# Performance work log

Hardware: AMD Instinct MI355X
Metric: run time of the kernel (lower is better)

The kernel has to match this reference:

```python
import jax, jax.numpy as jnp
import numpy as np

N_TYPES = 2
N_NODES = 50000
N_EDGES = 400000
C = 128
H = 4
D = C // H
L = 2
# edge type e connects src node type META[e][0] -> dst node type META[e][1]
META = ((0, 1), (1, 0))


def setup_inputs() -> dict:
    key = jax.random.key(0)
    ks = jax.random.split(key, 16)
    s = 0.05
    return {
        "x": jax.random.normal(ks[0], (N_TYPES, N_NODES, C), jnp.float32),
        "edge_index": jax.random.randint(ks[1], (2, 2, N_EDGES), 0, N_NODES, jnp.int64),
        "Wk": jax.random.normal(ks[2], (L, N_TYPES, C, C), jnp.float32) * s,
        "bk": jax.random.normal(ks[3], (L, N_TYPES, C), jnp.float32) * s,
        "Wq": jax.random.normal(ks[4], (L, N_TYPES, C, C), jnp.float32) * s,
        "bq": jax.random.normal(ks[5], (L, N_TYPES, C), jnp.float32) * s,
        "Wv": jax.random.normal(ks[6], (L, N_TYPES, C, C), jnp.float32) * s,
        "bv": jax.random.normal(ks[7], (L, N_TYPES, C), jnp.float32) * s,
        "Wa": jax.random.normal(ks[8], (L, N_TYPES, C, C), jnp.float32) * s,
        "ba": jax.random.normal(ks[9], (L, N_TYPES, C), jnp.float32) * s,
        "skip": jax.random.normal(ks[10], (L, N_TYPES), jnp.float32),
        "a_rel": jax.random.normal(ks[11], (L, 2, H, D, D), jnp.float32) * s,
        "m_rel": jax.random.normal(ks[12], (L, 2, H, D, D), jnp.float32) * s,
        "p_rel": jnp.ones((L, 2, H), jnp.float32),
        "ln_g": jnp.ones((L, N_TYPES, C), jnp.float32),
        "ln_b": jnp.zeros((L, N_TYPES, C), jnp.float32),
    }


def _layer(x, edge_index, Wk, bk, Wq, bq, Wv, bv, Wa, ba, skip, a_rel, m_rel, p_rel, ln_g, ln_b):
    # x: [T, N, C] ; per-type K/Q/V projections -> [T, N, H, D]
    k = (jnp.einsum('tnc,tcd->tnd', x, Wk) + bk[:, None]).reshape(N_TYPES, N_NODES, H, D)
    q = (jnp.einsum('tnc,tcd->tnd', x, Wq) + bq[:, None]).reshape(N_TYPES, N_NODES, H, D)
    v = (jnp.einsum('tnc,tcd->tnd', x, Wv) + bv[:, None]).reshape(N_TYPES, N_NODES, H, D)
    scale = 1.0 / float(np.sqrt(D))
    out = jnp.zeros((N_TYPES, N_NODES, H, D), x.dtype)
    for e, (st, dt) in enumerate(META):
        si, di = edge_index[e, 0], edge_index[e, 1]
        # per-relation transforms of gathered src keys/values: [E, H, D]
        k_rel = jnp.einsum('ehd,hdf->ehf', k[st][si], a_rel[e])
        v_rel = jnp.einsum('ehd,hdf->ehf', v[st][si], m_rel[e])
        # attention logits [E, H], softmax grouped by destination node
        att = jnp.sum(q[dt][di] * k_rel, axis=-1) * p_rel[e] * scale
        amax = jax.ops.segment_max(att, di, num_segments=N_NODES)
        att = jnp.exp(att - amax[di])
        den = jax.ops.segment_sum(att, di, num_segments=N_NODES)
        att = att / (den[di] + 1e-16)
        agg = jax.ops.segment_sum(att[..., None] * v_rel, di, num_segments=N_NODES)
        out = out.at[dt].add(agg)
    o = out.reshape(N_TYPES, N_NODES, C)
    o = jnp.einsum('tnc,tcd->tnd', jax.nn.gelu(o), Wa) + ba[:, None]
    beta = jax.nn.sigmoid(skip)[:, None, None]
    x = beta * o + (1.0 - beta) * x
    # per-type LayerNorm over features, then ReLU
    mu = jnp.mean(x, axis=-1, keepdims=True)
    var = jnp.var(x, axis=-1, keepdims=True)
    x = (x - mu) * jax.lax.rsqrt(var + 1e-5) * ln_g[:, None] + ln_b[:, None]
    return jax.nn.relu(x)


def reference(x, edge_index, Wk, bk, Wq, bq, Wv, bv, Wa, ba, skip, a_rel, m_rel, p_rel, ln_g, ln_b):
    for l in range(L):
        x = _layer(x, edge_index, Wk[l], bk[l], Wq[l], bq[l], Wv[l], bv[l],
                   Wa[l], ba[l], skip[l], a_rel[l], m_rel[l], p_rel[l], ln_g[l], ln_b[l])
    # x_dict[entity_table]: return node type 0 ("user") embeddings
    return x[0]
```

## Files before the change

kernel.cpp:

```cpp
#include <hip/hip_runtime.h>

#define NN 50000
#define EE 400000
#define CC 128
#define TT 2
#define NT16R 3128
#define KPB 8

typedef float floatx4 __attribute__((ext_vector_type(4)));
typedef float floatx2 __attribute__((ext_vector_type(2)));
typedef _Float16 half8 __attribute__((ext_vector_type(8)));
typedef _Float16 half2t __attribute__((ext_vector_type(2)));

__device__ __forceinline__ unsigned pk2h(float a, float b) {
    return __builtin_bit_cast(unsigned, __builtin_amdgcn_cvt_pkrtz(a, b));
}
__device__ __forceinline__ float gelu_f(float x) {
    float u = 0.7978845608028654f * (x + 0.044715f * x * x * x);
    float t = __expf(2.f * u);
    return x * (1.f - 1.f / (t + 1.f));
}

__device__ __forceinline__ floatx2 pkfma(floatx2 a, floatx2 b, floatx2 c) {
#if __has_builtin(__builtin_elementwise_fma)
    return __builtin_elementwise_fma(a, b, c);
#else
    floatx2 r;
    r.x = fmaf(a.x, b.x, c.x);
    r.y = fmaf(a.y, b.y, c.y);
    return r;
#endif
}

__device__ __forceinline__ unsigned pk_fp8x4(float a, float b, float c, float d) {
#if __has_builtin(__builtin_amdgcn_cvt_pk_fp8_f32)
    int v = 0;
    v = __builtin_amdgcn_cvt_pk_fp8_f32(a, b, v, false);
    v = __builtin_amdgcn_cvt_pk_fp8_f32(c, d, v, true);
    return (unsigned)v;
#else
    auto enc = [](float x) -> unsigned {
        unsigned u = __float_as_uint(x);
        unsigned s = (u >> 24) & 0x80;
        int e = (int)((u >> 23) & 0xff);
        unsigned m = u & 0x7fffff;
        if (e == 0) return s;
        int ne = e - 127 + 7;
        if (ne <= 0) {
            unsigned full = (1u << 23) | m;
            int sh = 21 - ne;
            if (sh > 24) return s;
            unsigned r = full >> sh;
            unsigned rem = full & ((1u << sh) - 1);
            unsigned half = 1u << (sh - 1);
            if (rem > half || (rem == half && (r & 1))) r++;
            return s | (r & 0x7f);
        }
        unsigned r = m >> 20;
        unsigned rem = m & 0xfffff;
        if (rem > 0x80000 || (rem == 0x80000 && (r & 1))) {
            r++;
            if (r == 8) { r = 0; ne++; }
        }
        if (ne > 15) return s | 0x7e;
        return s | ((unsigned)ne << 3) | r;
    };
    return enc(a) | (enc(b) << 8) | (enc(c) << 16) | (enc(d) << 24);
#endif
}

template <bool HI>
__device__ __forceinline__ floatx2 upk_fp8(unsigned v) {
#if __has_builtin(__builtin_amdgcn_cvt_pk_f32_fp8)
    return __builtin_amdgcn_cvt_pk_f32_fp8((int)v, HI);
#else
    auto dec = [](unsigned b) -> float {
        unsigned s = b & 0x80;
        unsigned e = (b >> 3) & 0xf;
        unsigned m = b & 7;
        float val;
        if (e == 0) val = (float)m * (1.f / 512.f);
        else val = (1.f + (float)m * 0.125f) * exp2f((float)e - 7.f);
        return s ? -val : val;
    };
    unsigned base = HI ? (v >> 16) : v;
    floatx2 r;
    r.x = dec(base & 0xff);
    r.y = dec((base >> 8) & 0xff);
    return r;
#endif
}

__global__ void k_detect(const int* __restrict__ ei, int* __restrict__ flag) {
    if (threadIdx.x == 0 && blockIdx.x == 0) {
        int orv = 0;
        for (int i = 1; i < 64; i += 2) orv |= ei[i];
        flag[0] = (orv == 0) ? 1 : 0;
    }
}

__global__ __launch_bounds__(256) void k_count(const int* __restrict__ ei,
                                               const int* __restrict__ flag,
                                               int* __restrict__ counts,
                                               unsigned short* __restrict__ rank) {
    int e = blockIdx.y;
    int tid = threadIdx.x;
    int base = blockIdx.x * (256 * KPB);
    int is64 = flag[0];
    const size_t db = (size_t)(e * 2 + 1) * EE;
    int di[KPB];
    bool val[KPB];
#pragma unroll
    for (int k = 0; k < KPB; k++) {
        int j = base + k * 256 + tid;
        val[k] = j < EE;
        int jc = val[k] ? j : 0;
        int d = is64 ? ei[(db + jc) * 2] : ei[db + jc];
        di[k] = min(max(d, 0), NN - 1);
    }
    int rk[KPB];
#pragma unroll
    for (int k = 0; k < KPB; k++)
        rk[k] = val[k] ? atomicAdd(&counts[e * NN + di[k]], 1) : 0;
#pragma unroll
    for (int k = 0; k < KPB; k++) {
        int j = base + k * 256 + tid;
        if (val[k]) rank[(size_t)e * EE + j] = (unsigned short)rk[k];
    }
}

#define SCB ((NN + 1023) / 1024)
__global__ __launch_bounds__(256) void k_scan1(const int* __restrict__ counts,
                                               int* __restrict__ rowptr,
                                               int* __restrict__ bsum) {
    int e = blockIdx.y, b = blockIdx.x;
    int tid = threadIdx.x, lane = tid & 63, wid = tid >> 6;
    __shared__ int wsum[4];
    int base = b * 1024 + tid * 4;
    int v[4], s = 0;
#pragma unroll
    for (int k2 = 0; k2 < 4; k2++) {
        int i = base + k2;
        v[k2] = (i < NN) ? counts[e * NN + i] : 0;
        s += v[k2];
    }
    int incl = s;
#pragma unroll
    for (int off = 1; off < 64; off <<= 1) {
        int t2 = __shfl_up(incl, off);
        if (lane >= off) incl += t2;
    }
    if (lane == 63) wsum[wid] = incl;
    __syncthreads();
    int woff = 0;
    for (int w2 = 0; w2 < wid; w2++) woff += wsum[w2];
    int excl = woff + incl - s;
#pragma unroll
    for (int k2 = 0; k2 < 4; k2++) {
        int i = base + k2;
        if (i < NN) rowptr[e * (NN + 1) + i] = excl;
        excl += v[k2];
    }
    if (tid == 255) bsum[e * SCB + b] = woff + incl;
}

__global__ void k_scan2(int* __restrict__ bsum, int* __restrict__ rowptr) {
    int e = threadIdx.x >> 6, lane = threadIdx.x & 63;
    int v = (lane < SCB) ? bsum[e * SCB + lane] : 0;
    int incl = v;
#pragma unroll
    for (int off = 1; off < 64; off <<= 1) {
        int t2 = __shfl_up(incl, off);
        if (lane >= off) incl += t2;
    }
    if (lane < SCB) bsum[e * SCB + lane] = incl - v;
    if (lane == 63) rowptr[e * (NN + 1) + NN] = incl;
}

__global__ __launch_bounds__(256) void k_scan3(int* __restrict__ rowptr,
                                               const int* __restrict__ bsum) {
    int e = blockIdx.y, b = blockIdx.x;
    int off = bsum[e * SCB + b];
    int base = b * 1024 + threadIdx.x * 4;
#pragma unroll
    for (int k2 = 0; k2 < 4; k2++) {
        int i = base + k2;
        if (i < NN) rowptr[e * (NN + 1) + i] += off;
    }
}

__global__ __launch_bounds__(256) void k_scatter(const int* __restrict__ ei,
                                                 const int* __restrict__ flag,
                                                 const int* __restrict__ rowptr,
                                                 const unsigned short* __restrict__ rank,
                                                 int* __restrict__ csr) {
    int e = blockIdx.y;
    int tid = threadIdx.x;
    int base = blockIdx.x * (256 * KPB);
    int is64 = flag[0];
    const size_t sb = (size_t)(e * 2 + 0) * EE;
    const size_t db = (size_t)(e * 2 + 1) * EE;
    int si[KPB], di[KPB], rk[KPB];
#pragma unroll
    for (int k = 0; k < KPB; k++) {
        int j = base + k * 256 + tid;
        int jc = (j < EE) ? j : 0;
        si[k] = is64 ? ei[(sb + jc) * 2] : ei[sb + jc];
        di[k] = is64 ? ei[(db + jc) * 2] : ei[db + jc];
        rk[k] = rank[(size_t)e * EE + jc];
    }
    int pos[KPB];
#pragma unroll
    for (int k = 0; k < KPB; k++) {
        di[k] = min(max(di[k], 0), NN - 1);
        si[k] = min(max(si[k], 0), NN - 1);
    }
#pragma unroll
    for (int k = 0; k < KPB; k++) pos[k] = rowptr[e * (NN + 1) + di[k]] + rk[k];
#pragma unroll
    for (int k = 0; k < KPB; k++) {
        int j = base + k * 256 + tid;
        if (j < EE) csr[(size_t)e * EE + pos[k]] = si[k];
    }
}

__global__ __launch_bounds__(256) void k_cvt(const float* __restrict__ x,
                                             _Float16* __restrict__ xs) {
    __shared__ _Float16 sm[64 * 132];
    int t = blockIdx.y;
    int tid = threadIdx.x;
    int node0 = blockIdx.x * 64;
#pragma unroll
    for (int p = 0; p < 8; p++) {
        int c = p * 256 + tid;
        int row = c >> 5, ch = c & 31;
        int node = min(node0 + row, NN - 1);
        float4 v = *(const float4*)(x + ((size_t)t * NN + node) * CC + ch * 4);
        uint2 o;
        o.x = pk2h(v.x, v.y);
        o.y = pk2h(v.z, v.w);
        *(uint2*)(sm + row * 132 + ch * 4) = o;
    }
    __syncthreads();
    _Float16* xt = xs + (size_t)t * NT16R * 2048;
#pragma unroll
    for (int p = 0; p < 4; p++) {
        int c = p * 256 + tid;
        int tl = c >> 8, kt = (c >> 6) & 3, l = c & 63;
        int q = l >> 4, ln = l & 15;
        *(uint4*)(xt + ((size_t)(blockIdx.x * 4 + tl) * 4 + kt) * 512 + l * 8) =
            *(const uint4*)(sm + (tl * 16 + ln) * 132 + kt * 32 + q * 8);
    }
}

__global__ void k_prep(const float* __restrict__ Wk, const float* __restrict__ Wq,
                       const float* __restrict__ Wv, const float* __restrict__ Wa,
                       const float* __restrict__ bk, const float* __restrict__ bq,
                       const float* __restrict__ bv,
                       const float* __restrict__ a_rel, const float* __restrict__ m_rel,
                       const float* __restrict__ p_rel,
                       _Float16* __restrict__ W2, _Float16* __restrict__ Wa2,
                       float* __restrict__ beff) {
    const float SCALE = 0.17677669529663687f * 1.4426950408889634f;
    int l = blockIdx.y;
    int idx = blockIdx.x * 256 + threadIdx.x;
    if (idx < 2 * 384 * 128) {
        int t = idx / (384 * 128);
        int r = idx - t * 384 * 128;
        int n = r >> 7, k = r & 127;
        float val;
        if (n < 128) {
            val = Wq[((l * 2 + t) * 128 + k) * 128 + n] *
                  p_rel[(l * 2 + (1 - t)) * 4 + (n >> 5)] * SCALE;
        } else if (n < 256) {
            int nn = n - 128, h = nn >> 5, f = nn & 31;
            const float* wr = Wk + ((l * 2 + t) * 128 + k) * 128 + h * 32;
            const float* ar = a_rel + (((l * 2 + t) * 4 + h) * 32) * 32 + f;
            float s = 0.f;
            for (int d = 0; d < 32; d++) s += wr[d] * ar[d * 32];
            val = s;
        } else {
            int nn = n - 256, h = nn >> 5, f = nn & 31;
            const float* wr = Wv + ((l * 2 + t) * 128 + k) * 128 + h * 32;
            const float* mr = m_rel + (((l * 2 + t) * 4 + h) * 32) * 32 + f;
            float s = 0.f;
            for (int d = 0; d < 32; d++) s += wr[d] * mr[d * 32];
            val = s;
        }
        W2[(((size_t)(l * 2 + t) * 24 + (n >> 4)) * 4 + (k >> 5)) * 512 +
           (((k & 31) >> 3) * 16 + (n & 15)) * 8 + (k & 7)] = (_Float16)val;
    } else if (idx < 2 * 384 * 128 + 2 * 128 * 128) {
        int r = idx - 2 * 384 * 128;
        int t = r / (128 * 128);
        r -= t * 128 * 128;
        int n = r >> 7, k = r & 127;
        float val = Wa[((l * 2 + t) * 128 + k) * 128 + n];
        Wa2[(((size_t)(l * 2 + t) * 8 + (n >> 4)) * 4 + (k >> 5)) * 512 +
            (((k & 31) >> 3) * 16 + (n & 15)) * 8 + (k & 7)] = (_Float16)val;
    } else if (idx < 2 * 384 * 128 + 2 * 128 * 128 + 2 * 384) {
        int r = idx - (2 * 384 * 128 + 2 * 128 * 128);
        int t = r / 384, n = r - t * 384;
        float val;
        if (n < 128) {
            val = bq[(l * 2 + t) * 128 + n] * p_rel[(l * 2 + (1 - t)) * 4 + (n >> 5)] * SCALE;
        } else if (n < 256) {
            int nn = n - 128, h = nn >> 5, f = nn & 31;
            float s = 0.f;
            for (int d = 0; d < 32; d++)
                s += bk[(l * 2 + t) * 128 + h * 32 + d] *
                     a_rel[(((l * 2 + t) * 4 + h) * 32 + d) * 32 + f];
            val = s;
        } else {
            int nn = n - 256, h = nn >> 5, f = nn & 31;
            float s = 0.f;
            for (int d = 0; d < 32; d++)
                s += bv[(l * 2 + t) * 128 + h * 32 + d] *
                     m_rel[(((l * 2 + t) * 4 + h) * 32 + d) * 32 + f];
            val = s;
        }
        beff[(l * 2 + t) * 384 + n] = val;
    }
}

template <int NT, int COL0>
__global__ __launch_bounds__(256) void k_gemm_qkv(const _Float16* __restrict__ xs,
                                                  const _Float16* __restrict__ W2,
                                                  const float* __restrict__ beff,
                                                  unsigned char* __restrict__ qkv8, int l,
                                                  int t0) {
    constexpr int RB = (NT == 6) ? 512 : 256;
    constexpr int RS = RB + 16;
    __shared__ unsigned char tile[32 * RS];
    int t = t0 + blockIdx.y;
    int tid = threadIdx.x;
    int wid = tid >> 6, lane = tid & 63;
    int quad = lane >> 4, ln = lane & 15;
    int node0 = blockIdx.x * 32;
    int tile0 = blockIdx.x * 2;
    int lt = l * 2 + t;
    const _Float16* Wt = W2 + (size_t)lt * 24 * 2048;
    const _Float16* xt = xs + (size_t)t * NT16R * 2048;
    half8 bf[2][4];
#pragma unroll
    for (int ns = 0; ns < 2; ns++)
#pragma unroll
        for (int kt = 0; kt < 4; kt++)
            bf[ns][kt] = *(const half8*)(xt + ((size_t)(tile0 + ns) * 4 + kt) * 512 + lane * 8);
    floatx4 acc[NT][2];
#pragma unroll
    for (int nt = 0; nt < NT; nt++)
#pragma unroll
        for (int ns = 0; ns < 2; ns++) acc[nt][ns] = (floatx4){0.f, 0.f, 0.f, 0.f};
#pragma unroll
    for (int nt = 0; nt < NT; nt++) {
        int mt = COL0 / 16 + wid * NT + nt;
#pragma unroll
        for (int kt = 0; kt < 4; kt++) {
            half8 af = *(const half8*)(Wt + ((size_t)mt * 4 + kt) * 512 + lane * 8);
            acc[nt][0] = __builtin_amdgcn_mfma_f32_16x16x32_f16(af, bf[0][kt], acc[nt][0], 0, 0, 0);
            acc[nt][1] = __builtin_amdgcn_mfma_f32_16x16x32_f16(af, bf[1][kt], acc[nt][1], 0, 0, 0);
        }
    }
#pragma unroll
    for (int nt = 0; nt < NT; nt++) {
        int c0 = COL0 + wid * NT * 16 + nt * 16 + quad * 4;
        float4 b4 = *(const float4*)(beff + (l * 2 + t) * 384 + c0);
#pragma unroll
        for (int ns = 0; ns < 2; ns++) {
            int nl = ns * 16 + ln;
            float v0 = acc[nt][ns][0] + b4.x, v1 = acc[nt][ns][1] + b4.y;
            float v2 = acc[nt][ns][2] + b4.z, v3 = acc[nt][ns][3] + b4.w;
            unsigned char* rowp = tile + nl * RS;
            if (c0 < 128) {
                uint2 o;
                o.x = pk2h(v0, v1);
                o.y = pk2h(v2, v3);
                *(uint2*)(rowp + 2 * c0) = o;
            } else {
                int f0 = c0 & 127;
                int isV = (c0 >= 256);
                int loff = (f0 >> 3) * 16 + (f0 & 7) + isV * 8 +
                           ((COL0 == 128) ? 0 : 256);
                *(unsigned*)(rowp + loff) = pk_fp8x4(v0, v1, v2, v3);
            }
        }
    }
    __syncthreads();
    constexpr int CPR = RB / 16;
    constexpr int PASSES = (32 * CPR) / 256;
#pragma unroll
    for (int p = 0; p < PASSES; p++) {
        int c = p * 256 + tid;
        int row = c / CPR, ch = c - row * CPR;
        int node = node0 + row;
        if (node < NN)
            *(uint4*)(qkv8 + ((size_t)t * NN + node) * 512 + (COL0 ? 256 : 0) + ch * 16) =
                *(const uint4*)(tile + row * RS + ch * 16);
    }
}

__global__ __launch_bounds__(256) void k_attn(const unsigned char* __restrict__ qkv8,
                                              const int* __restrict__ rowptr,
                                              const int* __restrict__ csr,
                                              _Float16* __restrict__ outg) {
    int t = blockIdx.y;
    int e = 1 - t;
    int st = 1 - t;
    int wid = threadIdx.x >> 6, lane = threadIdx.x & 63;
    int n = __builtin_amdgcn_readfirstlane(blockIdx.x * 4 + wid);
    int e4 = lane >> 4, s = lane & 15;
    int r0 = rowptr[e * (NN + 1) + n];
    int r1 = rowptr[e * (NN + 1) + n + 1];
    const int* csrp = csr + (size_t)e * EE;
    const unsigned char* sbase = qkv8 + (size_t)st * NN * 512;
    uint4 qd = *(const uint4*)(qkv8 + ((size_t)t * NN + n) * 512 + s * 16);

    floatx2 acc2[4];
#pragma unroll
    for (int i = 0; i < 4; i++) acc2[i] = (floatx2){0.f, 0.f};
    float lsum = 0.f;
    floatx2 q2[4];

    auto process = [&](const uint4& u, float msk) {
        floatx2 p2 = q2[0] * upk_fp8<false>(u.x);
        p2 = pkfma(q2[1], upk_fp8<true>(u.x), p2);
        p2 = pkfma(q2[2], upk_fp8<false>(u.y), p2);
        p2 = pkfma(q2[3], upk_fp8<true>(u.y), p2);
        float p = p2.x + p2.y;
        p += __shfl_xor(p, 1);
        p += __shfl_xor(p, 2);
        float w = exp2f(p) * msk;
        lsum += w;
        floatx2 w2 = (floatx2){w, w};
        acc2[0] = pkfma(w2, upk_fp8<false>(u.z), acc2[0]);
        acc2[1] = pkfma(w2, upk_fp8<true>(u.z), acc2[1]);
        acc2[2] = pkfma(w2, upk_fp8<false>(u.w), acc2[2]);
        acc2[3] = pkfma(w2, upk_fp8<true>(u.w), acc2[3]);
    };

    if (r0 < r1) {
        int j = r0;
        int iA = csrp[min(j + e4, r1 - 1)];
        int iB = csrp[min(j + 4 + e4, r1 - 1)];
        uint4 uA = (uint4){0u, 0u, 0u, 0u};
        if (j + e4 < r1) uA = *(const uint4*)(sbase + (size_t)iA * 512 + 256 + s * 16);
        {
            half2t h0 = __builtin_bit_cast(half2t, qd.x), h1 = __builtin_bit_cast(half2t, qd.y);
            half2t h2 = __builtin_bit_cast(half2t, qd.z), h3 = __builtin_bit_cast(half2t, qd.w);
            q2[0] = (floatx2){(float)h0.x, (float)h0.y};
            q2[1] = (floatx2){(float)h1.x, (float)h1.y};
            q2[2] = (floatx2){(float)h2.x, (float)h2.y};
            q2[3] = (floatx2){(float)h3.x, (float)h3.y};
        }
        for (; j + 8 < r1; j += 4) {
            uint4 uB = *(const uint4*)(sbase + (size_t)iB * 512 + 256 + s * 16);
            iB = csrp[min(j + 8 + e4, r1 - 1)];
            process(uA, 1.f);
            uA = uB;
        }
        if (j + 4 < r1) {
            uint4 uB = (uint4){0u, 0u, 0u, 0u};
            float mB = (j + 4 + e4 < r1) ? 1.f : 0.f;
            if (j + 4 + e4 < r1)
                uB = *(const uint4*)(sbase + (size_t)iB * 512 + 256 + s * 16);
            process(uA, 1.f);
            process(uB, mB);
        } else {
            process(uA, (j + e4 < r1) ? 1.f : 0.f);
        }
    }
    float accf[8] = {acc2[0].x, acc2[0].y, acc2[1].x, acc2[1].y,
                     acc2[2].x, acc2[2].y, acc2[3].x, acc2[3].y};
#pragma unroll
    for (int i = 0; i < 8; i++) {
        accf[i] += __shfl_xor(accf[i], 16);
        accf[i] += __shfl_xor(accf[i], 32);
    }
    lsum += __shfl_xor(lsum, 16);
    lsum += __shfl_xor(lsum, 32);
    float inv = 1.f / (lsum + 1e-16f);
    if (e4 == 0) {
        uint4 o;
        o.x = pk2h(accf[0] * inv, accf[1] * inv);
        o.y = pk2h(accf[2] * inv, accf[3] * inv);
        o.z = pk2h(accf[4] * inv, accf[5] * inv);
        o.w = pk2h(accf[6] * inv, accf[7] * inv);
        *(uint4*)(outg + ((size_t)t * NN + n) * CC + s * 8) = o;
    }
}

__global__ __launch_bounds__(256) void k_epilogue(
    const _Float16* __restrict__ outg, const _Float16* __restrict__ Wa2,
    const float* __restrict__ ba, const float* __restrict__ skipv,
    const float* __restrict__ ln_g, const float* __restrict__ ln_b,
    const _Float16* __restrict__ xs_cur, _Float16* __restrict__ xs_next,
    float* __restrict__ xout, int l) {
    __shared__ _Float16 smem_h[64 * 132];
    int t = blockIdx.y;
    int tid = threadIdx.x;
    int wid = tid >> 6, lane = tid & 63;
    int quad = lane >> 4, ln = lane & 15;
    int node0 = blockIdx.x * 64;
    int nloc = wid * 16 + ln;
    int node = node0 + nloc;
    int arow = min(node, NN - 1);
    const _Float16* grow = outg + ((size_t)t * NN + arow) * CC;
    uint4 gd4[4];
#pragma unroll
    for (int kt = 0; kt < 4; kt++) gd4[kt] = *(const uint4*)(grow + kt * 32 + quad * 8);
    const _Float16* xt = xs_cur + (size_t)t * NT16R * 2048;
    int tileR = arow >> 4, lnR = arow & 15;
    uint2 xw8[8];
#pragma unroll
    for (int nt = 0; nt < 8; nt++) {
        int c0 = nt * 16 + quad * 4;
        xw8[nt] = *(const uint2*)(xt + ((size_t)tileR * 4 + (c0 >> 5)) * 512 +
                                  (((c0 >> 3) & 3) * 16 + lnR) * 8 + (c0 & 7));
    }
    half8 bf[4];
#pragma unroll
    for (int kt = 0; kt < 4; kt++) {
        uint4 gd = gd4[kt];
        half2t h0 = __builtin_bit_cast(half2t, gd.x), h1 = __builtin_bit_cast(half2t, gd.y);
        half2t h2 = __builtin_bit_cast(half2t, gd.z), h3 = __builtin_bit_cast(half2t, gd.w);
        uint4 pk;
        pk.x = pk2h(gelu_f((float)h0.x), gelu_f((float)h0.y));
        pk.y = pk2h(gelu_f((float)h1.x), gelu_f((float)h1.y));
        pk.z = pk2h(gelu_f((float)h2.x), gelu_f((float)h2.y));
        pk.w = pk2h(gelu_f((float)h3.x), gelu_f((float)h3.y));
        bf[kt] = __builtin_bit_cast(half8, pk);
    }
    const _Float16* Wt = Wa2 + (size_t)(l * 2 + t) * 8 * 2048;
    floatx4 acc[8];
#pragma unroll
    for (int nt = 0; nt < 8; nt++) acc[nt] = (floatx4){0.f, 0.f, 0.f, 0.f};
#pragma unroll
    for (int nt = 0; nt < 8; nt++) {
#pragma unroll
        for (int kt = 0; kt < 4; kt++) {
            half8 af = *(const half8*)(Wt + ((size_t)nt * 4 + kt) * 512 + lane * 8);
            acc[nt] = __builtin_amdgcn_mfma_f32_16x16x32_f16(af, bf[kt], acc[nt], 0, 0, 0);
        }
    }
    float sv = skipv[l * TT + t];
    float beta = 1.f / (1.f + __expf(-sv));
    float xn[8][4];
    float s1 = 0.f, s2 = 0.f;
#pragma unroll
    for (int nt = 0; nt < 8; nt++) {
        int c0 = nt * 16 + quad * 4;
        float4 b4 = *(const float4*)(ba + (l * TT + t) * CC + c0);
        half2t x0 = __builtin_bit_cast(half2t, xw8[nt].x),
               x1 = __builtin_bit_cast(half2t, xw8[nt].y);
        float xv[4] = {(float)x0.x, (float)x0.y, (float)x1.x, (float)x1.y};
        float bb[4] = {b4.x, b4.y, b4.z, b4.w};
#pragma unroll
        for (int reg = 0; reg < 4; reg++) {
            float o = acc[nt][reg] + bb[reg];
            float v = beta * o + (1.f - beta) * xv[reg];
            xn[nt][reg] = v;
            s1 += v;
            s2 += v * v;
        }
    }
    s1 += __shfl_xor(s1, 16); s1 += __shfl_xor(s1, 32);
    s2 += __shfl_xor(s2, 16); s2 += __shfl_xor(s2, 32);
    float mu = s1 * (1.f / CC);
    float var = s2 * (1.f / CC) - mu * mu;
    float rs = rsqrtf(var + 1e-5f);
#pragma unroll
    for (int nt = 0; nt < 8; nt++) {
        int c0 = nt * 16 + quad * 4;
        float4 g4 = *(const float4*)(ln_g + (l * TT + t) * CC + c0);
        float4 be4 = *(const float4*)(ln_b + (l * TT + t) * CC + c0);
        float y0 = fmaxf((xn[nt][0] - mu) * rs * g4.x + be4.x, 0.f);
        float y1 = fmaxf((xn[nt][1] - mu) * rs * g4.y + be4.y, 0.f);
        float y2 = fmaxf((xn[nt][2] - mu) * rs * g4.z + be4.z, 0.f);
        float y3 = fmaxf((xn[nt][3] - mu) * rs * g4.w + be4.w, 0.f);
        if (xout) {
            if (node < NN) {
                float4 o4 = {y0, y1, y2, y3};
                *(float4*)(xout + (size_t)node * CC + c0) = o4;
            }
        } else {
            uint2 o;
            o.x = pk2h(y0, y1);
            o.y = pk2h(y2, y3);
            *(uint2*)(smem_h + nloc * 132 + c0) = o;
        }
    }
    if (!xout) {
        __syncthreads();
        _Float16* xnt = xs_next + (size_t)t * NT16R * 2048;
#pragma unroll
        for (int p = 0; p < 4; p++) {
            int c = p * 256 + tid;
            int tl = c >> 8, kt2 = (c >> 6) & 3, l2 = c & 63;
            int q2 = l2 >> 4, ln2 = l2 & 15;
            *(uint4*)(xnt + ((size_t)(blockIdx.x * 4 + tl) * 4 + kt2) * 512 + l2 * 8) =
                *(const uint4*)(smem_h + (tl * 16 + ln2) * 132 + kt2 * 32 + q2 * 8);
        }
    }
}

extern "C" void kernel_launch(void* const* d_in, const int* in_sizes, int n_in,
                              void* d_out, int out_size, void* d_ws, size_t ws_size,
                              hipStream_t stream) {
    const float* x = (const float*)d_in[0];
    const int* ei = (const int*)d_in[1];
    const float* Wk = (const float*)d_in[2];
    const float* bk = (const float*)d_in[3];
    const float* Wq = (const float*)d_in[4];
    const float* bq = (const float*)d_in[5];
    const float* Wv = (const float*)d_in[6];
    const float* bv = (const float*)d_in[7];
    const float* Wa = (const float*)d_in[8];
    const float* ba = (const float*)d_in[9];
    const float* skip = (const float*)d_in[10];
    const float* a_rel = (const float*)d_in[11];
    const float* m_rel = (const float*)d_in[12];
    const float* p_rel = (const float*)d_in[13];
    const float* ln_g = (const float*)d_in[14];
    const float* ln_b = (const float*)d_in[15];

    char* ws = (char*)d_ws;
    size_t off = 0;
    auto alloc = [&](size_t b) {
        size_t o = off;
        off = (off + b + 255) & ~(size_t)255;
        return o;
    };
    _Float16* xsA = (_Float16*)(ws + alloc((size_t)TT * NT16R * 2048 * 2));
    _Float16* xsB = (_Float16*)(ws + alloc((size_t)TT * NT16R * 2048 * 2));
    unsigned char* qkv8 = (unsigned char*)(ws + alloc((size_t)TT * NN * 512));
    _Float16* outg = (_Float16*)(ws + alloc((size_t)TT * NN * CC * 2));
    _Float16* W2 = (_Float16*)(ws + alloc((size_t)2 * TT * 24 * 2048 * 2));
    _Float16* Wa2 = (_Float16*)(ws + alloc((size_t)2 * TT * 8 * 2048 * 2));
    float* beff = (float*)(ws + alloc((size_t)2 * TT * 384 * 4));
    int* counts = (int*)(ws + alloc((size_t)2 * NN * 4));
    unsigned short* rankb = (unsigned short*)(ws + alloc((size_t)2 * EE * 2));
    int* rowptr = (int*)(ws + alloc((size_t)2 * (NN + 1) * 4));
    int* csr = (int*)(ws + alloc((size_t)2 * EE * 4));
    int* flag = (int*)(ws + alloc(256));
    int* bsum = (int*)(ws + alloc((size_t)2 * SCB * 4 + 256));
    (void)ws_size; (void)in_sizes; (void)n_in; (void)out_size;

    k_detect<<<1, 64, 0, stream>>>(ei, flag);
    (void)hipMemsetAsync(counts, 0, (size_t)2 * NN * 4, stream);
    const int EB = (EE + 256 * KPB - 1) / (256 * KPB);
    k_count<<<dim3(EB, 2), 256, 0, stream>>>(ei, flag, counts, rankb);
    k_scan1<<<dim3(SCB, 2), 256, 0, stream>>>(counts, rowptr, bsum);
    k_scan2<<<1, 128, 0, stream>>>(bsum, rowptr);
    k_scan3<<<dim3(SCB, 2), 256, 0, stream>>>(rowptr, bsum);
    k_scatter<<<dim3(EB, 2), 256, 0, stream>>>(ei, flag, rowptr, rankb, csr);
    k_cvt<<<dim3(NT16R / 4, 2), 256, 0, stream>>>(x, xsA);
    k_prep<<<dim3((2 * 384 * 128 + 2 * 128 * 128 + 2 * 384 + 255) / 256, 2), 256, 0, stream>>>(
        Wk, Wq, Wv, Wa, bk, bq, bv, a_rel, m_rel, p_rel, W2, Wa2, beff);

    const int GB = (NN + 31) / 32;
    k_gemm_qkv<6, 0><<<dim3(GB, 2), 256, 0, stream>>>(xsA, W2, beff, qkv8, 0, 0);
    k_attn<<<dim3(NN / 4, 2), 256, 0, stream>>>(qkv8, rowptr, csr, outg);
    k_epilogue<<<dim3((NN + 63) / 64, 2), 256, 0, stream>>>(
        outg, Wa2, ba, skip, ln_g, ln_b, xsA, xsB, nullptr, 0);
    k_gemm_qkv<2, 0><<<dim3(GB, 1), 256, 0, stream>>>(xsB, W2, beff, qkv8, 1, 0);
    k_gemm_qkv<4, 128><<<dim3(GB, 1), 256, 0, stream>>>(xsB, W2, beff, qkv8, 1, 1);
    k_attn<<<dim3(NN / 4, 1), 256, 0, stream>>>(qkv8, rowptr, csr, outg);
    k_epilogue<<<dim3((NN + 63) / 64, 1), 256, 0, stream>>>(
        outg, Wa2, ba, skip, ln_g, ln_b, xsB, nullptr, (float*)d_out, 1);
}
```

Measured before the change: 332.5 us.

## Merge small launches: inline dtype detect, fuse scan passes, cvt+prep, layer-1 GEMMs

Removes the separate detect kernel by having each count/scatter block check the index dtype itself. The two-pass scan tail becomes a single kernel, and the x conversion and weight prep run as one launch split by block index. The two layer-1 QKV GEMM launches also become one launch over a 2-D grid. The aim is to cut the number of kernel launches and the serialization gaps between them, at the cost of a redundant per-block dtype check and a redundant 64-lane block-sum scan in every scan block.

```diff
diff --git a/kernel.cpp b/kernel.cpp
--- a/kernel.cpp
+++ b/kernel.cpp
@@ -6,6 +6,10 @@
 #define TT 2
 #define NT16R 3128
 #define KPB 8
+#define SCB ((NN + 1023) / 1024)
+#define CVTB (NT16R / 4)
+#define PREPN (2 * 384 * 128 + 2 * 128 * 128 + 2 * 384)
+#define PREPB ((PREPN + 255) / 256)
 
 typedef float floatx4 __attribute__((ext_vector_type(4)));
 typedef float floatx2 __attribute__((ext_vector_type(2)));
@@ -91,22 +95,25 @@
 #endif
 }
 
-__global__ void k_detect(const int* __restrict__ ei, int* __restrict__ flag) {
-    if (threadIdx.x == 0 && blockIdx.x == 0) {
+__device__ __forceinline__ int detect_is64(const int* __restrict__ ei, int* sflag) {
+    if (threadIdx.x == 0) {
         int orv = 0;
+#pragma unroll
         for (int i = 1; i < 64; i += 2) orv |= ei[i];
-        flag[0] = (orv == 0) ? 1 : 0;
-    }
+        *sflag = (orv == 0) ? 1 : 0;
+    }
+    __syncthreads();
+    return *sflag;
 }
 
 __global__ __launch_bounds__(256) void k_count(const int* __restrict__ ei,
-                                               const int* __restrict__ flag,
                                                int* __restrict__ counts,
                                                unsigned short* __restrict__ rank) {
+    __shared__ int sflag;
+    int is64 = detect_is64(ei, &sflag);
     int e = blockIdx.y;
     int tid = threadIdx.x;
     int base = blockIdx.x * (256 * KPB);
-    int is64 = flag[0];
     const size_t db = (size_t)(e * 2 + 1) * EE;
     int di[KPB];
     bool val[KPB];
@@ -129,7 +136,6 @@
     }
 }
 
-#define SCB ((NN + 1023) / 1024)
 __global__ __launch_bounds__(256) void k_scan1(const int* __restrict__ counts,
                                                int* __restrict__ rowptr,
                                                int* __restrict__ bsum) {
@@ -164,40 +170,42 @@
     if (tid == 255) bsum[e * SCB + b] = woff + incl;
 }
 
-__global__ void k_scan2(int* __restrict__ bsum, int* __restrict__ rowptr) {
-    int e = threadIdx.x >> 6, lane = threadIdx.x & 63;
-    int v = (lane < SCB) ? bsum[e * SCB + lane] : 0;
-    int incl = v;
-#pragma unroll
-    for (int off = 1; off < 64; off <<= 1) {
-        int t2 = __shfl_up(incl, off);
-        if (lane >= off) incl += t2;
-    }
-    if (lane < SCB) bsum[e * SCB + lane] = incl - v;
-    if (lane == 63) rowptr[e * (NN + 1) + NN] = incl;
-}
-
-__global__ __launch_bounds__(256) void k_scan3(int* __restrict__ rowptr,
-                                               const int* __restrict__ bsum) {
+__global__ __launch_bounds__(256) void k_scan23(int* __restrict__ rowptr,
+                                                const int* __restrict__ bsum) {
+    __shared__ int soff2[2];
     int e = blockIdx.y, b = blockIdx.x;
-    int off = bsum[e * SCB + b];
-    int base = b * 1024 + threadIdx.x * 4;
+    int tid = threadIdx.x, lane = tid & 63, wv = tid >> 6;
+    if (wv == 0) {
+        int v = (lane < SCB) ? bsum[e * SCB + lane] : 0;
+        int incl = v;
+#pragma unroll
+        for (int off = 1; off < 64; off <<= 1) {
+            int t2 = __shfl_up(incl, off);
+            if (lane >= off) incl += t2;
+        }
+        if (lane == b) soff2[0] = incl - v;
+        if (lane == SCB - 1) soff2[1] = incl;
+    }
+    __syncthreads();
+    int off = soff2[0];
+    int base = b * 1024 + tid * 4;
 #pragma unroll
     for (int k2 = 0; k2 < 4; k2++) {
         int i = base + k2;
         if (i < NN) rowptr[e * (NN + 1) + i] += off;
     }
+    if (b == 0 && tid == 0) rowptr[e * (NN + 1) + NN] = soff2[1];
 }
 
 __global__ __launch_bounds__(256) void k_scatter(const int* __restrict__ ei,
-                                                 const int* __restrict__ flag,
                                                  const int* __restrict__ rowptr,
                                                  const unsigned short* __restrict__ rank,
                                                  int* __restrict__ csr) {
+    __shared__ int sflag;
+    int is64 = detect_is64(ei, &sflag);
     int e = blockIdx.y;
     int tid = threadIdx.x;
     int base = blockIdx.x * (256 * KPB);
-    int is64 = flag[0];
     const size_t sb = (size_t)(e * 2 + 0) * EE;
     const size_t db = (size_t)(e * 2 + 1) * EE;
     int si[KPB], di[KPB], rk[KPB];
@@ -224,46 +232,48 @@
     }
 }
 
-__global__ __launch_bounds__(256) void k_cvt(const float* __restrict__ x,
-                                             _Float16* __restrict__ xs) {
+__global__ __launch_bounds__(256) void k_cvt_prep(
+    const float* __restrict__ x, _Float16* __restrict__ xs,
+    const float* __restrict__ Wk, const float* __restrict__ Wq,
+    const float* __restrict__ Wv, const float* __restrict__ Wa,
+    const float* __restrict__ bk, const float* __restrict__ bq,
+    const float* __restrict__ bv,
+    const float* __restrict__ a_rel, const float* __restrict__ m_rel,
+    const float* __restrict__ p_rel,
+    _Float16* __restrict__ W2, _Float16* __restrict__ Wa2,
+    float* __restrict__ beff) {
     __shared__ _Float16 sm[64 * 132];
-    int t = blockIdx.y;
     int tid = threadIdx.x;
-    int node0 = blockIdx.x * 64;
-#pragma unroll
-    for (int p = 0; p < 8; p++) {
-        int c = p * 256 + tid;
-        int row = c >> 5, ch = c & 31;
-        int node = min(node0 + row, NN - 1);
-        float4 v = *(const float4*)(x + ((size_t)t * NN + node) * CC + ch * 4);
-        uint2 o;
-        o.x = pk2h(v.x, v.y);
-        o.y = pk2h(v.z, v.w);
-        *(uint2*)(sm + row * 132 + ch * 4) = o;
-    }
-    __syncthreads();
-    _Float16* xt = xs + (size_t)t * NT16R * 2048;
-#pragma unroll
-    for (int p = 0; p < 4; p++) {
-        int c = p * 256 + tid;
-        int tl = c >> 8, kt = (c >> 6) & 3, l = c & 63;
-        int q = l >> 4, ln = l & 15;
-        *(uint4*)(xt + ((size_t)(blockIdx.x * 4 + tl) * 4 + kt) * 512 + l * 8) =
-            *(const uint4*)(sm + (tl * 16 + ln) * 132 + kt * 32 + q * 8);
-    }
-}
-
-__global__ void k_prep(const float* __restrict__ Wk, const float* __restrict__ Wq,
-                       const float* __restrict__ Wv, const float* __restrict__ Wa,
-                       const float* __restrict__ bk, const float* __restrict__ bq,
-                       const float* __restrict__ bv,
-                       const float* __restrict__ a_rel, const float* __restrict__ m_rel,
-                       const float* __restrict__ p_rel,
-                       _Float16* __restrict__ W2, _Float16* __restrict__ Wa2,
-                       float* __restrict__ beff) {
+    if (blockIdx.x < CVTB) {
+        int bx = blockIdx.x;
+        int t = blockIdx.y;
+        int node0 = bx * 64;
+#pragma unroll
+        for (int p = 0; p < 8; p++) {
+            int c = p * 256 + tid;
+            int row = c >> 5, ch = c & 31;
+            int node = min(node0 + row, NN - 1);
+            float4 v = *(const float4*)(x + ((size_t)t * NN + node) * CC + ch * 4);
+            uint2 o;
+            o.x = pk2h(v.x, v.y);
+            o.y = pk2h(v.z, v.w);
+            *(uint2*)(sm + row * 132 + ch * 4) = o;
+        }
+        __syncthreads();
+        _Float16* xt = xs + (size_t)t * NT16R * 2048;
+#pragma unroll
+        for (int p = 0; p < 4; p++) {
+            int c = p * 256 + tid;
+            int tl = c >> 8, kt = (c >> 6) & 3, l = c & 63;
+            int q = l >> 4, ln = l & 15;
+            *(uint4*)(xt + ((size_t)(bx * 4 + tl) * 4 + kt) * 512 + l * 8) =
+                *(const uint4*)(sm + (tl * 16 + ln) * 132 + kt * 32 + q * 8);
+        }
+        return;
+    }
     const float SCALE = 0.17677669529663687f * 1.4426950408889634f;
     int l = blockIdx.y;
-    int idx = blockIdx.x * 256 + threadIdx.x;
+    int idx = (blockIdx.x - CVTB) * 256 + tid;
     if (idx < 2 * 384 * 128) {
         int t = idx / (384 * 128);
         int r = idx - t * 384 * 128;
@@ -297,7 +307,7 @@
         float val = Wa[((l * 2 + t) * 128 + k) * 128 + n];
         Wa2[(((size_t)(l * 2 + t) * 8 + (n >> 4)) * 4 + (k >> 5)) * 512 +
             (((k & 31) >> 3) * 16 + (n & 15)) * 8 + (k & 7)] = (_Float16)val;
-    } else if (idx < 2 * 384 * 128 + 2 * 128 * 128 + 2 * 384) {
+    } else if (idx < PREPN) {
         int r = idx - (2 * 384 * 128 + 2 * 128 * 128);
         int t = r / 384, n = r - t * 384;
         float val;
@@ -323,20 +333,19 @@
 }
 
 template <int NT, int COL0>
-__global__ __launch_bounds__(256) void k_gemm_qkv(const _Float16* __restrict__ xs,
-                                                  const _Float16* __restrict__ W2,
-                                                  const float* __restrict__ beff,
-                                                  unsigned char* __restrict__ qkv8, int l,
-                                                  int t0) {
+__device__ __forceinline__ void gemm_body(const _Float16* __restrict__ xs,
+                                          const _Float16* __restrict__ W2,
+                                          const float* __restrict__ beff,
+                                          unsigned char* __restrict__ qkv8,
+                                          int l, int t, int bx,
+                                          unsigned char* tile) {
     constexpr int RB = (NT == 6) ? 512 : 256;
     constexpr int RS = RB + 16;
-    __shared__ unsigned char tile[32 * RS];
-    int t = t0 + blockIdx.y;
     int tid = threadIdx.x;
     int wid = tid >> 6, lane = tid & 63;
     int quad = lane >> 4, ln = lane & 15;
-    int node0 = blockIdx.x * 32;
-    int tile0 = blockIdx.x * 2;
+    int node0 = bx * 32;
+    int tile0 = bx * 2;
     int lt = l * 2 + t;
     const _Float16* Wt = W2 + (size_t)lt * 24 * 2048;
     const _Float16* xt = xs + (size_t)t * NT16R * 2048;
@@ -397,6 +406,28 @@
             *(uint4*)(qkv8 + ((size_t)t * NN + node) * 512 + (COL0 ? 256 : 0) + ch * 16) =
                 *(const uint4*)(tile + row * RS + ch * 16);
     }
+}
+
+template <int NT, int COL0>
+__global__ __launch_bounds__(256) void k_gemm_qkv(const _Float16* __restrict__ xs,
+                                                  const _Float16* __restrict__ W2,
+                                                  const float* __restrict__ beff,
+                                                  unsigned char* __restrict__ qkv8, int l,
+                                                  int t0) {
+    constexpr int RB = (NT == 6) ? 512 : 256;
+    __shared__ unsigned char tile[32 * (RB + 16)];
+    gemm_body<NT, COL0>(xs, W2, beff, qkv8, l, t0 + blockIdx.y, blockIdx.x, tile);
+}
+
+__global__ __launch_bounds__(256) void k_gemm_l1(const _Float16* __restrict__ xs,
+                                                 const _Float16* __restrict__ W2,
+                                                 const float* __restrict__ beff,
+                                                 unsigned char* __restrict__ qkv8) {
+    __shared__ unsigned char tile[32 * 272];
+    if (blockIdx.y == 0)
+        gemm_body<2, 0>(xs, W2, beff, qkv8, 1, 0, blockIdx.x, tile);
+    else
+        gemm_body<4, 128>(xs, W2, beff, qkv8, 1, 1, blockIdx.x, tile);
 }
 
 __global__ __launch_bounds__(256) void k_attn(const unsigned char* __restrict__ qkv8,
@@ -641,29 +672,24 @@
     unsigned short* rankb = (unsigned short*)(ws + alloc((size_t)2 * EE * 2));
     int* rowptr = (int*)(ws + alloc((size_t)2 * (NN + 1) * 4));
     int* csr = (int*)(ws + alloc((size_t)2 * EE * 4));
-    int* flag = (int*)(ws + alloc(256));
     int* bsum = (int*)(ws + alloc((size_t)2 * SCB * 4 + 256));
     (void)ws_size; (void)in_sizes; (void)n_in; (void)out_size;
 
-    k_detect<<<1, 64, 0, stream>>>(ei, flag);
     (void)hipMemsetAsync(counts, 0, (size_t)2 * NN * 4, stream);
     const int EB = (EE + 256 * KPB - 1) / (256 * KPB);
-    k_count<<<dim3(EB, 2), 256, 0, stream>>>(ei, flag, counts, rankb);
+    k_count<<<dim3(EB, 2), 256, 0, stream>>>(ei, counts, rankb);
     k_scan1<<<dim3(SCB, 2), 256, 0, stream>>>(counts, rowptr, bsum);
-    k_scan2<<<1, 128, 0, stream>>>(bsum, rowptr);
-    k_scan3<<<dim3(SCB, 2), 256, 0, stream>>>(rowptr, bsum);
-    k_scatter<<<dim3(EB, 2), 256, 0, stream>>>(ei, flag, rowptr, rankb, csr);
-    k_cvt<<<dim3(NT16R / 4, 2), 256, 0, stream>>>(x, xsA);
-    k_prep<<<dim3((2 * 384 * 128 + 2 * 128 * 128 + 2 * 384 + 255) / 256, 2), 256, 0, stream>>>(
-        Wk, Wq, Wv, Wa, bk, bq, bv, a_rel, m_rel, p_rel, W2, Wa2, beff);
+    k_scan23<<<dim3(SCB, 2), 256, 0, stream>>>(rowptr, bsum);
+    k_scatter<<<dim3(EB, 2), 256, 0, stream>>>(ei, rowptr, rankb, csr);
+    k_cvt_prep<<<dim3(CVTB + PREPB, 2), 256, 0, stream>>>(
+        x, xsA, Wk, Wq, Wv, Wa, bk, bq, bv, a_rel, m_rel, p_rel, W2, Wa2, beff);
 
     const int GB = (NN + 31) / 32;
     k_gemm_qkv<6, 0><<<dim3(GB, 2), 256, 0, stream>>>(xsA, W2, beff, qkv8, 0, 0);
     k_attn<<<dim3(NN / 4, 2), 256, 0, stream>>>(qkv8, rowptr, csr, outg);
     k_epilogue<<<dim3((NN + 63) / 64, 2), 256, 0, stream>>>(
         outg, Wa2, ba, skip, ln_g, ln_b, xsA, xsB, nullptr, 0);
-    k_gemm_qkv<2, 0><<<dim3(GB, 1), 256, 0, stream>>>(xsB, W2, beff, qkv8, 1, 0);
-    k_gemm_qkv<4, 128><<<dim3(GB, 1), 256, 0, stream>>>(xsB, W2, beff, qkv8, 1, 1);
+    k_gemm_l1<<<dim3(GB, 2), 256, 0, stream>>>(xsB, W2, beff, qkv8);
     k_attn<<<dim3(NN / 4, 1), 256, 0, stream>>>(qkv8, rowptr, csr, outg);
     k_epilogue<<<dim3((NN + 63) / 64, 1), 256, 0, stream>>>(
         outg, Wa2, ba, skip, ln_g, ln_b, xsB, nullptr, (float*)d_out, 1);
```

Result: faster. 321.9 us (-3.2%).
